# Kernel tuning notes

Hardware: AMD Instinct MI355X
Metric: run time of the kernel (lower is better)

The kernel has to match this reference:

```python
import jax, jax.numpy as jnp
import numpy as np

D = 512
H = 4 * D
EPS = 1e-5

def layernorm(x, g, b):
    mu = jnp.mean(x, axis=-1, keepdims=True)
    var = jnp.mean((x - mu) ** 2, axis=-1, keepdims=True)
    return (x - mu) * jax.lax.rsqrt(var + EPS) * g + b

def setup_inputs() -> dict:
    key = jax.random.key(0)
    ks = jax.random.split(key, 16)
    s = 0.02
    inp = {
        "x": jax.random.normal(ks[0], (16, 2048, D), dtype=jnp.float32),
        "wq": jax.random.normal(ks[1], (D, D), dtype=jnp.float32) * s,
        "bq": jnp.zeros((D,), jnp.float32),
        "wk": jax.random.normal(ks[2], (D, D), dtype=jnp.float32) * s,
        "bk": jnp.zeros((D,), jnp.float32),
        "wv": jax.random.normal(ks[3], (D, D), dtype=jnp.float32) * s,
        "bv": jnp.zeros((D,), jnp.float32),
        "wp": jax.random.normal(ks[4], (D, D), dtype=jnp.float32) * s,
        "bp": jnp.zeros((D,), jnp.float32),
        "w1": jax.random.normal(ks[5], (D, H), dtype=jnp.float32) * s,
        "b1": jnp.zeros((H,), jnp.float32),
        "w2": jax.random.normal(ks[6], (H, D), dtype=jnp.float32) * s,
        "b2": jnp.zeros((D,), jnp.float32),
        "g1": jnp.ones((D,), jnp.float32),
        "be1": jnp.zeros((D,), jnp.float32),
        "g2": jnp.ones((D,), jnp.float32),
        "be2": jnp.zeros((D,), jnp.float32),
    }
    return inp

def reference(x, wq, bq, wk, bk, wv, bv, wp, bp, w1, b1, w2, b2, g1, be1, g2, be2):
    temperature = jnp.sqrt(jnp.asarray(D, x.dtype))
    q = x @ wq + bq                      # [B,N,D]
    k = x @ wk + bk
    v = x @ wv + bv
    energy = jnp.einsum('bnd,bmd->bnm', q / temperature, k)   # [B,N,N]
    attn = jax.nn.softmax(energy, axis=-1)
    out = jnp.einsum('bnm,bmd->bnd', attn, v)
    att = out @ wp + bp
    x = layernorm(x + att, g1, be1)
    h = jax.nn.gelu(x @ w1 + b1, approximate=False)
    ff = h @ w2 + b2
    x = layernorm(x + ff, g2, be2)
    return x
```

## Files before the change

### kernel.cpp

```cpp
#include <hip/hip_runtime.h>
#include <cmath>

typedef __bf16 bf16_t;
typedef __bf16 bf16x8 __attribute__((ext_vector_type(8)));
typedef __bf16 bf16x4 __attribute__((ext_vector_type(4)));
typedef float f32x4 __attribute__((ext_vector_type(4)));

#define DEV_INLINE __device__ __forceinline__

DEV_INLINE void gload_lds16(const void* g, void* l) {
  __builtin_amdgcn_global_load_lds(
      (const __attribute__((address_space(1))) void*)g,
      (__attribute__((address_space(3))) void*)l, 16, 0, 0);
}

DEV_INLINE float gelu_f(float v) {
  const float u = v * (0.7978845608f + 0.0356774081f * v * v);
  const float e = __expf(2.f * u);
  const float th = 1.f - 2.f / (e + 1.f);
  return 0.5f * v * (1.f + th);
}

template<int EPI, bool HAS_BIAS>
__global__ __launch_bounds__(512, 1)
void gemm256(const bf16_t* __restrict__ A, const bf16_t* __restrict__ B,
             const float* __restrict__ bias, void* __restrict__ C,
             bf16_t* __restrict__ vTaux,
             int M, int N, int K, int lda, int ldb, int ldc,
             long sA, long sB, long sC, float scale)
{
  __shared__ alignas(16) bf16_t As[2][16384];
  __shared__ alignas(16) bf16_t Bs[2][16384];
  const int b = blockIdx.z;
  A += (long)b * sA;
  B += (long)b * sB;
  const int t  = threadIdx.x;
  const int l  = t & 63;
  const int w  = t >> 6;
  const int wm = w >> 2;
  const int wn = w & 3;
  const int m0 = blockIdx.y * 256;
  const int n0 = blockIdx.x * 256;

  const int srow  = t >> 3;
  const int scolb = ((t & 7) * 16) ^ ((srow & 7) << 4);
  const bf16_t* gA = A + (long)(m0 + srow) * lda + (scolb >> 1);
  const bf16_t* gB = B + (long)(n0 + srow) * ldb + (scolb >> 1);

  const int fr = l & 15;
  const int kq = l >> 4;
  int offA[8][2], offB[4][2];
#pragma unroll
  for (int mi = 0; mi < 8; mi++) {
    const int row = wm * 128 + mi * 16 + fr;
    const int swz = (row & 7) << 4;
#pragma unroll
    for (int ks = 0; ks < 2; ks++)
      offA[mi][ks] = row * 64 + (((ks * 64 + kq * 16) ^ swz) >> 1);
  }
#pragma unroll
  for (int ni = 0; ni < 4; ni++) {
    const int row = wn * 64 + ni * 16 + fr;
    const int swz = (row & 7) << 4;
#pragma unroll
    for (int ks = 0; ks < 2; ks++)
      offB[ni][ks] = row * 64 + (((ks * 64 + kq * 16) ^ swz) >> 1);
  }

#define STAGE256(kt, q) do {                                          \
    const long ko_ = (long)(kt) * 64;                                 \
    gload_lds16(gA + ko_,                    &As[q][t * 8]);          \
    gload_lds16(gA + 64  * (long)lda + ko_,  &As[q][4096  + t * 8]);  \
    gload_lds16(gA + 128 * (long)lda + ko_,  &As[q][8192  + t * 8]);  \
    gload_lds16(gA + 192 * (long)lda + ko_,  &As[q][12288 + t * 8]);  \
    gload_lds16(gB + ko_,                    &Bs[q][t * 8]);          \
    gload_lds16(gB + 64  * (long)ldb + ko_,  &Bs[q][4096  + t * 8]);  \
    gload_lds16(gB + 128 * (long)ldb + ko_,  &Bs[q][8192  + t * 8]);  \
    gload_lds16(gB + 192 * (long)ldb + ko_,  &Bs[q][12288 + t * 8]);  \
  } while (0)

  f32x4 acc[8][4] = {};

  const int NT = K >> 6;
  STAGE256(0, 0);
  __syncthreads();

  int cur = 0;
  for (int kt = 0; kt < NT; ++kt) {
    if (kt + 1 < NT) STAGE256(kt + 1, cur ^ 1);
#pragma unroll
    for (int ks = 0; ks < 2; ks++) {
      bf16x8 af[8], bf[4];
#pragma unroll
      for (int mi = 0; mi < 8; mi++)
        af[mi] = *(const bf16x8*)&As[cur][offA[mi][ks]];
#pragma unroll
      for (int ni = 0; ni < 4; ni++)
        bf[ni] = *(const bf16x8*)&Bs[cur][offB[ni][ks]];
#pragma unroll
      for (int mi = 0; mi < 8; mi++)
#pragma unroll
        for (int ni = 0; ni < 4; ni++)
          acc[mi][ni] = __builtin_amdgcn_mfma_f32_16x16x32_bf16(
              af[mi], bf[ni], acc[mi][ni], 0, 0, 0);
    }
    __syncthreads();
    cur ^= 1;
  }
#undef STAGE256

  const long cb = (long)b * sC;
  const int rbase = m0 + wm * 128 + kq * 4;
#pragma unroll
  for (int mi = 0; mi < 8; mi++) {
    const int row0 = rbase + mi * 16;
#pragma unroll
    for (int ni = 0; ni < 4; ni++) {
      const int c = n0 + wn * 64 + ni * 16 + fr;
      float bias_v = 0.f;
      if constexpr (HAS_BIAS) bias_v = bias[c];
      float vals[4];
#pragma unroll
      for (int r = 0; r < 4; r++) {
        float v = acc[mi][ni][r] + bias_v;
        if constexpr (EPI == 2) v *= scale;
        if constexpr (EPI == 3) v = gelu_f(v);
        vals[r] = v;
      }
      if constexpr (EPI == 5) {
        if (c < 1024) {
#pragma unroll
          for (int r = 0; r < 4; r++)
            ((bf16_t*)C)[(long)(row0 + r) * ldc + c] = (bf16_t)vals[r];
        } else {
          const int bb = row0 >> 11;
          const int n  = row0 & 2047;
          bf16x4 pk = { (bf16_t)vals[0], (bf16_t)vals[1],
                        (bf16_t)vals[2], (bf16_t)vals[3] };
          *(bf16x4*)&vTaux[(long)bb * (512 * 2048) + (long)(c - 1024) * 2048 + n] = pk;
        }
      } else {
#pragma unroll
        for (int r = 0; r < 4; r++) {
          const long idx = cb + (long)(row0 + r) * ldc + c;
          if constexpr (EPI == 0) ((float*)C)[idx] = vals[r];
          else                    ((bf16_t*)C)[idx] = (bf16_t)vals[r];
        }
      }
    }
  }
}

template<int EPI, bool HAS_BIAS>
__global__ __launch_bounds__(256, 2)
void gemm_bt(const bf16_t* __restrict__ A, const bf16_t* __restrict__ B,
             const float* __restrict__ bias, void* __restrict__ C,
             bf16_t* __restrict__ vTaux,
             int M, int N, int K, int lda, int ldb, int ldc,
             long sA, long sB, long sC, float scale)
{
  __shared__ alignas(16) bf16_t lds[3][2][4096];
  const int b = blockIdx.z;
  A += (long)b * sA;
  B += (long)b * sB;
  const int t  = threadIdx.x;
  const int l  = t & 63;
  const int w  = t >> 6;
  const int wr = (w >> 1) * 64;
  const int wc = (w & 1) * 64;
  const int m0 = blockIdx.y * 128;
  const int n0 = blockIdx.x * 128;

  const int r0 = t >> 2;
  const int r1 = r0 + 64;
  const int wb = (t & 3) * 16;
  const int cb0 = wb ^ (((r0 >> 1) & 3) << 4);
  const int cb1 = wb ^ (((r1 >> 1) & 3) << 4);
  const bf16_t* gA0 = A + (long)(m0 + r0) * lda + (cb0 >> 1);
  const bf16_t* gA1 = A + (long)(m0 + r1) * lda + (cb1 >> 1);
  const bf16_t* gB0 = B + (long)(n0 + r0) * ldb + (cb0 >> 1);
  const bf16_t* gB1 = B + (long)(n0 + r1) * ldb + (cb1 >> 1);

#define STAGE(kt, q) do {                                   \
    const long kofs_ = (long)(kt) * 32;                     \
    gload_lds16(gA0 + kofs_, &lds[q][0][t * 8]);            \
    gload_lds16(gA1 + kofs_, &lds[q][0][2048 + t * 8]);     \
    gload_lds16(gB0 + kofs_, &lds[q][1][t * 8]);            \
    gload_lds16(gB1 + kofs_, &lds[q][1][2048 + t * 8]);     \
  } while (0)

  const int fr  = l & 15;
  const int kkb = (l >> 4) * 16;
  int offA[4], offB[4];
#pragma unroll
  for (int mi = 0; mi < 4; mi++) {
    const int row = wr + mi * 16 + fr;
    offA[mi] = row * 32 + ((kkb ^ (((row >> 1) & 3) << 4)) >> 1);
  }
#pragma unroll
  for (int ni = 0; ni < 4; ni++) {
    const int row = wc + ni * 16 + fr;
    offB[ni] = row * 32 + ((kkb ^ (((row >> 1) & 3) << 4)) >> 1);
  }

  f32x4 acc[4][4] = {};

  const int NT = K >> 5;
  STAGE(0, 0);
  STAGE(1, 1);

  int q = 0;
  for (int kt = 0; kt < NT; ++kt) {
    if (kt < NT - 1) asm volatile("s_waitcnt vmcnt(4)" ::: "memory");
    else             asm volatile("s_waitcnt vmcnt(0)" ::: "memory");
    __builtin_amdgcn_sched_barrier(0);
    __builtin_amdgcn_s_barrier();

    if (kt + 2 < NT) {
      int qs = q + 2; if (qs >= 3) qs -= 3;
      STAGE(kt + 2, qs);
    }

    bf16x8 af[4], bfr[4];
#pragma unroll
    for (int mi = 0; mi < 4; mi++)
      af[mi] = *(const bf16x8*)&lds[q][0][offA[mi]];
#pragma unroll
    for (int ni = 0; ni < 4; ni++)
      bfr[ni] = *(const bf16x8*)&lds[q][1][offB[ni]];
#pragma unroll
    for (int mi = 0; mi < 4; mi++)
#pragma unroll
      for (int ni = 0; ni < 4; ni++)
        acc[mi][ni] = __builtin_amdgcn_mfma_f32_16x16x32_bf16(
            af[mi], bfr[ni], acc[mi][ni], 0, 0, 0);

    if (++q == 3) q = 0;
  }
#undef STAGE

  const long cb = (long)b * sC;
  const int rbase = m0 + wr + (l >> 4) * 4;
#pragma unroll
  for (int mi = 0; mi < 4; mi++) {
    const int row0 = rbase + mi * 16;
#pragma unroll
    for (int ni = 0; ni < 4; ni++) {
      const int c = n0 + wc + ni * 16 + fr;
      float bias_v = 0.f;
      if constexpr (HAS_BIAS) bias_v = bias[c];
      float vals[4];
#pragma unroll
      for (int r = 0; r < 4; r++) {
        float v = acc[mi][ni][r] + bias_v;
        if constexpr (EPI == 2) v *= scale;
        if constexpr (EPI == 3) v = gelu_f(v);
        vals[r] = v;
      }
#pragma unroll
      for (int r = 0; r < 4; r++) {
        const long idx = cb + (long)(row0 + r) * ldc + c;
        if constexpr (EPI == 0) ((float*)C)[idx] = vals[r];
        else                    ((bf16_t*)C)[idx] = (bf16_t)vals[r];
      }
    }
  }
}

__global__ __launch_bounds__(256)
void transpose_cast(const float* __restrict__ in, bf16_t* __restrict__ out,
                    int R, int Cc)
{
  __shared__ float tile[32][33];
  const int c0 = blockIdx.x * 32;
  const int r0 = blockIdx.y * 32;
  const int tx = threadIdx.x & 31;
  const int ty = threadIdx.x >> 5;
#pragma unroll
  for (int i = 0; i < 32; i += 8)
    tile[ty + i][tx] = in[(long)(r0 + ty + i) * Cc + (c0 + tx)];
  __syncthreads();
#pragma unroll
  for (int i = 0; i < 32; i += 8)
    out[(long)(c0 + ty + i) * R + (r0 + tx)] = (bf16_t)tile[tx][ty + i];
}

__global__ __launch_bounds__(256)
void cast_to_bf16(const float* __restrict__ in, bf16_t* __restrict__ out, long n)
{
  const long i = ((long)blockIdx.x * 256 + threadIdx.x) * 4;
  if (i >= n) return;
  const float4 v = *(const float4*)&in[i];
  bf16x4 o = { (bf16_t)v.x, (bf16_t)v.y, (bf16_t)v.z, (bf16_t)v.w };
  *(bf16x4*)&out[i] = o;
}

__global__ __launch_bounds__(256)
void concat_bias(const float* __restrict__ a, const float* __restrict__ b,
                 const float* __restrict__ c, float* __restrict__ o)
{
  const int i = blockIdx.x * 256 + threadIdx.x;
  if (i < 512) o[i] = a[i];
  else if (i < 1024) o[i] = b[i - 512];
  else if (i < 1536) o[i] = c[i - 1024];
}

__global__ __launch_bounds__(256)
void softmax2048(bf16_t* __restrict__ E)
{
  const long row = blockIdx.x;
  bf16_t* p = E + row * 2048;
  const int t = threadIdx.x;
  bf16x8 xv = *(const bf16x8*)&p[t * 8];
  float v[8];
#pragma unroll
  for (int j = 0; j < 8; j++) v[j] = (float)xv[j];
  float m = v[0];
#pragma unroll
  for (int j = 1; j < 8; j++) m = fmaxf(m, v[j]);
  for (int o = 32; o; o >>= 1) m = fmaxf(m, __shfl_xor(m, o));
  __shared__ float redm[4];
  __shared__ float reds[4];
  if ((t & 63) == 0) redm[t >> 6] = m;
  __syncthreads();
  m = fmaxf(fmaxf(redm[0], redm[1]), fmaxf(redm[2], redm[3]));
  float s = 0.f;
#pragma unroll
  for (int j = 0; j < 8; j++) { v[j] = __expf(v[j] - m); s += v[j]; }
  for (int o = 32; o; o >>= 1) s += __shfl_xor(s, o);
  if ((t & 63) == 0) reds[t >> 6] = s;
  __syncthreads();
  s = reds[0] + reds[1] + reds[2] + reds[3];
  const float inv = 1.f / s;
  bf16x8 ov;
#pragma unroll
  for (int j = 0; j < 8; j++) ov[j] = (bf16_t)(v[j] * inv);
  *(bf16x8*)&p[t * 8] = ov;
}

template<bool A_BF16, bool EMIT_F32, bool EMIT_BF16>
__global__ __launch_bounds__(128)
void add_ln(const void* __restrict__ xa_, const float* __restrict__ xadd,
            const float* __restrict__ g, const float* __restrict__ be,
            float* __restrict__ y, bf16_t* __restrict__ yb)
{
  const long row = blockIdx.x;
  const int c = threadIdx.x * 4;
  float av[4];
  if constexpr (A_BF16) {
    const bf16_t* xa = (const bf16_t*)xa_;
    bf16x4 a = *(const bf16x4*)&xa[row * 512 + c];
#pragma unroll
    for (int j = 0; j < 4; j++) av[j] = (float)a[j];
  } else {
    const float* xa = (const float*)xa_;
    const float4 a = *(const float4*)&xa[row * 512 + c];
    av[0] = a.x; av[1] = a.y; av[2] = a.z; av[3] = a.w;
  }
  const float4 bb = *(const float4*)&xadd[row * 512 + c];
  float vv[4] = { av[0] + bb.x, av[1] + bb.y, av[2] + bb.z, av[3] + bb.w };
  float s = 0.f, s2 = 0.f;
#pragma unroll
  for (int j = 0; j < 4; j++) { s += vv[j]; s2 += vv[j] * vv[j]; }
  for (int o = 32; o; o >>= 1) { s += __shfl_xor(s, o); s2 += __shfl_xor(s2, o); }
  __shared__ float r0[2], r1[2];
  const int w = threadIdx.x >> 6;
  if ((threadIdx.x & 63) == 0) { r0[w] = s; r1[w] = s2; }
  __syncthreads();
  s = r0[0] + r0[1]; s2 = r1[0] + r1[1];
  const float mu = s * (1.f / 512.f);
  const float var = s2 * (1.f / 512.f) - mu * mu;
  const float rstd = rsqrtf(var + 1e-5f);
  const float4 gg = *(const float4*)&g[c];
  const float4 bev = *(const float4*)&be[c];
  float o0 = (vv[0] - mu) * rstd * gg.x + bev.x;
  float o1 = (vv[1] - mu) * rstd * gg.y + bev.y;
  float o2 = (vv[2] - mu) * rstd * gg.z + bev.z;
  float o3 = (vv[3] - mu) * rstd * gg.w + bev.w;
  if constexpr (EMIT_F32) {
    float4 yo = { o0, o1, o2, o3 };
    *(float4*)&y[row * 512 + c] = yo;
  }
  if constexpr (EMIT_BF16) {
    bf16x4 ob = { (bf16_t)o0, (bf16_t)o1, (bf16_t)o2, (bf16_t)o3 };
    *(bf16x4*)&yb[row * 512 + c] = ob;
  }
}

extern "C" void kernel_launch(void* const* d_in, const int* in_sizes, int n_in,
                              void* d_out, int out_size, void* d_ws, size_t ws_size,
                              hipStream_t stream)
{
  const float* x   = (const float*)d_in[0];
  const float* wq  = (const float*)d_in[1];
  const float* bq  = (const float*)d_in[2];
  const float* wk  = (const float*)d_in[3];
  const float* bk  = (const float*)d_in[4];
  const float* wv  = (const float*)d_in[5];
  const float* bv  = (const float*)d_in[6];
  const float* wp  = (const float*)d_in[7];
  const float* bp  = (const float*)d_in[8];
  const float* w1  = (const float*)d_in[9];
  const float* b1  = (const float*)d_in[10];
  const float* w2  = (const float*)d_in[11];
  const float* b2  = (const float*)d_in[12];
  const float* g1  = (const float*)d_in[13];
  const float* be1 = (const float*)d_in[14];
  const float* g2  = (const float*)d_in[15];
  const float* be2 = (const float*)d_in[16];

  const long S = 16L * 2048 * 512;
  const long Mi = 1L << 20;

  const size_t NEED = (size_t)200 * Mi;
  if (ws_size < NEED) return;

  char* wsp = (char*)d_ws;
  bf16_t* wqkvT = (bf16_t*)(wsp + 0);
  bf16_t* wpT   = wqkvT + 1536L * 512;
  bf16_t* w1T   = wpT + 512L * 512;
  bf16_t* w2T   = w1T + 2048L * 512;
  float*  bqkv  = (float*)(w2T + 512L * 2048);
  bf16_t* xb  = (bf16_t*)(wsp +   8 * Mi);
  bf16_t* qkb = (bf16_t*)(wsp +  40 * Mi);
  bf16_t* vT  = (bf16_t*)(wsp + 104 * Mi);
  bf16_t* E   = (bf16_t*)(wsp + 136 * Mi);
  bf16_t* ob  = xb;
  bf16_t* x1b = qkb;
  bf16_t* h   = (bf16_t*)(wsp + 72 * Mi);

  cast_to_bf16<<<dim3((unsigned)(S / 4 / 256)), 256, 0, stream>>>(x, xb, S);

  transpose_cast<<<dim3(16, 16), 256, 0, stream>>>(wq, wqkvT,               512, 512);
  transpose_cast<<<dim3(16, 16), 256, 0, stream>>>(wk, wqkvT + 512L * 512,  512, 512);
  transpose_cast<<<dim3(16, 16), 256, 0, stream>>>(wv, wqkvT + 1024L * 512, 512, 512);
  transpose_cast<<<dim3(16, 16), 256, 0, stream>>>(wp, wpT, 512, 512);
  transpose_cast<<<dim3(64, 16), 256, 0, stream>>>(w1, w1T, 512, 2048);
  transpose_cast<<<dim3(16, 64), 256, 0, stream>>>(w2, w2T, 2048, 512);
  concat_bias<<<dim3(6), 256, 0, stream>>>(bq, bk, bv, bqkv);

  gemm256<5, true><<<dim3(6, 128, 1), 512, 0, stream>>>(
      xb, wqkvT, bqkv, qkb, vT, 32768, 1536, 512, 512, 512, 1024, 0, 0, 0, 0.f);

  for (int cgrp = 0; cgrp < 2; cgrp++) {
    const long qoff = (long)cgrp * 8 * 2048 * 1024;
    gemm256<2, false><<<dim3(8, 8, 8), 512, 0, stream>>>(
        qkb + qoff, qkb + qoff + 512, nullptr, E, nullptr,
        2048, 2048, 512, 1024, 1024, 2048,
        2048L * 1024, 2048L * 1024, 2048L * 2048, 0.04419417382f);
    softmax2048<<<dim3(16384), 256, 0, stream>>>(E);
    gemm_bt<1, false><<<dim3(4, 16, 8), 256, 0, stream>>>(
        E, vT + (long)cgrp * 8 * 512 * 2048, nullptr,
        ob + (long)cgrp * 8 * 2048 * 512, nullptr,
        2048, 512, 2048, 2048, 2048, 512,
        2048L * 2048, 512L * 2048, 2048L * 512, 0.f);
  }

  gemm256<0, true><<<dim3(2, 128, 1), 512, 0, stream>>>(
      ob, wpT, bp, (float*)d_out, nullptr,
      32768, 512, 512, 512, 512, 512, 0, 0, 0, 0.f);

  add_ln<false, false, true><<<dim3(32768), 128, 0, stream>>>(
      x, (float*)d_out, g1, be1, nullptr, x1b);

  gemm256<3, true><<<dim3(8, 128, 1), 512, 0, stream>>>(
      x1b, w1T, b1, h, nullptr, 32768, 2048, 512, 512, 512, 2048, 0, 0, 0, 0.f);

  gemm256<0, true><<<dim3(2, 128, 1), 512, 0, stream>>>(
      h, w2T, b2, (float*)d_out, nullptr,
      32768, 512, 2048, 2048, 2048, 512, 0, 0, 0, 0.f);

  add_ln<true, true, false><<<dim3(32768), 128, 0, stream>>>(
      x1b, (float*)d_out, g2, be2, (float*)d_out, nullptr);
}
```

Measured before the change: 655.3 us.

## Interleave GEMM LDS reads, MFMA quadrants and split global loads with barriers

Restructures the 256x256 GEMM main loop into a two-k-tile unrolled iteration. Each iteration computes four quadrants of the accumulator, and the global-to-LDS loads for half-tiles are spread between them. The loop uses explicit s_barrier, lgkmcnt/vmcnt waits, sched_barrier and s_setprio to overlap memory traffic with MFMA work, in the style of HipKittens-type ping-pong scheduling. It assumes the k-tile count is even and relies on carefully chosen vmcnt values, so any mismatch risks a correctness race.

```diff
diff --git a/kernel.cpp b/kernel.cpp
--- a/kernel.cpp
+++ b/kernel.cpp
@@ -47,6 +47,17 @@
   const bf16_t* gA = A + (long)(m0 + srow) * lda + (scolb >> 1);
   const bf16_t* gB = B + (long)(n0 + srow) * ldb + (scolb >> 1);
 
+#define SG_A(q, h, kt) do { const long ko_ = (long)(kt) * 64;                 \
+    gload_lds16(gA + (long)((h) * 128) * lda + ko_,                           \
+                &As[q][(h) * 8192 + t * 8]);                                  \
+    gload_lds16(gA + (long)((h) * 128 + 64) * lda + ko_,                      \
+                &As[q][(h) * 8192 + 4096 + t * 8]); } while (0)
+#define SG_B(q, h, kt) do { const long ko_ = (long)(kt) * 64;                 \
+    gload_lds16(gB + (long)((h) * 128) * ldb + ko_,                           \
+                &Bs[q][(h) * 8192 + t * 8]);                                  \
+    gload_lds16(gB + (long)((h) * 128 + 64) * ldb + ko_,                      \
+                &Bs[q][(h) * 8192 + 4096 + t * 8]); } while (0)
+
   const int fr = l & 15;
   const int kq = l >> 4;
   int offA[8][2], offB[4][2];
@@ -67,47 +78,105 @@
       offB[ni][ks] = row * 64 + (((ks * 64 + kq * 16) ^ swz) >> 1);
   }
 
-#define STAGE256(kt, q) do {                                          \
-    const long ko_ = (long)(kt) * 64;                                 \
-    gload_lds16(gA + ko_,                    &As[q][t * 8]);          \
-    gload_lds16(gA + 64  * (long)lda + ko_,  &As[q][4096  + t * 8]);  \
-    gload_lds16(gA + 128 * (long)lda + ko_,  &As[q][8192  + t * 8]);  \
-    gload_lds16(gA + 192 * (long)lda + ko_,  &As[q][12288 + t * 8]);  \
-    gload_lds16(gB + ko_,                    &Bs[q][t * 8]);          \
-    gload_lds16(gB + 64  * (long)ldb + ko_,  &Bs[q][4096  + t * 8]);  \
-    gload_lds16(gB + 128 * (long)ldb + ko_,  &Bs[q][8192  + t * 8]);  \
-    gload_lds16(gB + 192 * (long)ldb + ko_,  &Bs[q][12288 + t * 8]);  \
+#define RD_A(arr, q, mh) do {                                                 \
+  _Pragma("unroll") for (int mi2_ = 0; mi2_ < 4; ++mi2_) {                    \
+    arr[mi2_][0] = *(const bf16x8*)&As[q][offA[(mh) * 4 + mi2_][0]];          \
+    arr[mi2_][1] = *(const bf16x8*)&As[q][offA[(mh) * 4 + mi2_][1]]; } } while (0)
+#define RD_B(arr, q, nh) do {                                                 \
+  _Pragma("unroll") for (int ni2_ = 0; ni2_ < 2; ++ni2_) {                    \
+    arr[ni2_][0] = *(const bf16x8*)&Bs[q][offB[(nh) * 2 + ni2_][0]];          \
+    arr[ni2_][1] = *(const bf16x8*)&Bs[q][offB[(nh) * 2 + ni2_][1]]; } } while (0)
+#define MM(mh, nh, AA, BB)                                                    \
+  _Pragma("unroll") for (int mi2_ = 0; mi2_ < 4; ++mi2_)                      \
+  _Pragma("unroll") for (int ni2_ = 0; ni2_ < 2; ++ni2_)                      \
+  _Pragma("unroll") for (int ks_ = 0; ks_ < 2; ++ks_)                         \
+    acc[(mh) * 4 + mi2_][(nh) * 2 + ni2_] =                                   \
+        __builtin_amdgcn_mfma_f32_16x16x32_bf16(                              \
+            AA[mi2_][ks_], BB[ni2_][ks_],                                     \
+            acc[(mh) * 4 + mi2_][(nh) * 2 + ni2_], 0, 0, 0);
+
+#define BAR()   __builtin_amdgcn_s_barrier()
+#define LGKM0() do { asm volatile("s_waitcnt lgkmcnt(0)" ::: "memory");       \
+                     __builtin_amdgcn_sched_barrier(0); } while (0)
+#define PRIO1() __builtin_amdgcn_s_setprio(1)
+#define PRIO0() do { __builtin_amdgcn_s_setprio(0);                           \
+                     __builtin_amdgcn_sched_barrier(0); } while (0)
+
+  f32x4 acc[8][4] = {};
+  bf16x8 a0[4][2], a1[4][2], b0[2][2], b1[2][2];
+
+  const int NT = K >> 6;
+  const int NITER = NT >> 1;
+
+  SG_A(0, 0, 0); SG_A(0, 1, 0); SG_B(0, 0, 0); SG_B(0, 1, 0);
+  SG_B(1, 0, 1); SG_B(1, 1, 1); SG_A(1, 0, 1);
+  asm volatile("s_waitcnt vmcnt(6)" ::: "memory");
+  __builtin_amdgcn_sched_barrier(0);
+  BAR();
+
+#define GEMM256_ITER(LAST, k0) do {                                           \
+                          \
+    RD_A(a0, 0, 0); RD_B(b0, 0, 0);                                           \
+    SG_A(1, 1, (k0) + 1);                       \
+    BAR(); LGKM0();                                                           \
+    PRIO1(); MM(0, 0, a0, b0) PRIO0(); BAR();                                 \
+                                                     \
+    RD_B(b1, 0, 1);                                                           \
+    BAR(); LGKM0();                                                           \
+    PRIO1(); MM(0, 1, a0, b1) PRIO0(); BAR();                                 \
+      \
+    RD_A(a1, 0, 1);                                                           \
+    if (!(LAST)) { SG_B(0, 0, (k0) + 2); SG_B(0, 1, (k0) + 2); }              \
+    BAR(); LGKM0();                                                           \
+    PRIO1(); MM(1, 0, a1, b0) PRIO0(); BAR();                                 \
+            \
+    if (!(LAST)) {                                                            \
+      SG_A(0, 0, (k0) + 2);                                                   \
+      asm volatile("s_waitcnt vmcnt(6)" ::: "memory");                        \
+    } else {                                                                  \
+      asm volatile("s_waitcnt vmcnt(0)" ::: "memory");                        \
+    }                                                                         \
+    __builtin_amdgcn_sched_barrier(0);                                        \
+    BAR();                                                                    \
+    PRIO1(); MM(1, 1, a1, b1) PRIO0(); BAR();                                 \
+               \
+    RD_A(a0, 1, 0); RD_B(b0, 1, 0);                                           \
+    if (!(LAST)) SG_A(0, 1, (k0) + 2);                                        \
+    BAR(); LGKM0();                                                           \
+    PRIO1(); MM(0, 0, a0, b0) PRIO0(); BAR();                                 \
+                                                     \
+    RD_B(b1, 1, 1);                                                           \
+    BAR(); LGKM0();                                                           \
+    PRIO1(); MM(0, 1, a0, b1) PRIO0(); BAR();                                 \
+                              \
+    RD_A(a1, 1, 1);                                                           \
+    if (!(LAST)) { SG_B(1, 0, (k0) + 3); SG_B(1, 1, (k0) + 3); }              \
+    BAR(); LGKM0();                                                           \
+    PRIO1(); MM(1, 0, a1, b0) PRIO0(); BAR();                                 \
+            \
+    if (!(LAST)) {                                                            \
+      SG_A(1, 0, (k0) + 3);                                                   \
+      asm volatile("s_waitcnt vmcnt(6)" ::: "memory");                        \
+      __builtin_amdgcn_sched_barrier(0);                                      \
+    }                                                                         \
+    BAR();                                                                    \
+    PRIO1(); MM(1, 1, a1, b1) PRIO0(); BAR();                                 \
   } while (0)
 
-  f32x4 acc[8][4] = {};
-
-  const int NT = K >> 6;
-  STAGE256(0, 0);
-  __syncthreads();
-
-  int cur = 0;
-  for (int kt = 0; kt < NT; ++kt) {
-    if (kt + 1 < NT) STAGE256(kt + 1, cur ^ 1);
-#pragma unroll
-    for (int ks = 0; ks < 2; ks++) {
-      bf16x8 af[8], bf[4];
-#pragma unroll
-      for (int mi = 0; mi < 8; mi++)
-        af[mi] = *(const bf16x8*)&As[cur][offA[mi][ks]];
-#pragma unroll
-      for (int ni = 0; ni < 4; ni++)
-        bf[ni] = *(const bf16x8*)&Bs[cur][offB[ni][ks]];
-#pragma unroll
-      for (int mi = 0; mi < 8; mi++)
-#pragma unroll
-        for (int ni = 0; ni < 4; ni++)
-          acc[mi][ni] = __builtin_amdgcn_mfma_f32_16x16x32_bf16(
-              af[mi], bf[ni], acc[mi][ni], 0, 0, 0);
-    }
-    __syncthreads();
-    cur ^= 1;
-  }
-#undef STAGE256
+  for (int tt = 0; tt < NITER - 1; ++tt)
+    GEMM256_ITER(0, 2 * tt);
+  GEMM256_ITER(1, NT - 2);
+
+#undef GEMM256_ITER
+#undef SG_A
+#undef SG_B
+#undef RD_A
+#undef RD_B
+#undef MM
+#undef BAR
+#undef LGKM0
+#undef PRIO1
+#undef PRIO0
 
   const long cb = (long)b * sC;
   const int rbase = m0 + wm * 128 + kq * 4;
```

New measurement: 643.4 us. No clear change (-1.8%).
